# Performance work log

Hardware: AMD Instinct MI355X
Metric: run time of the kernel (lower is better)

Reference implementation:

```python
import jax, jax.numpy as jnp
import numpy as np

B, S, D = 2, 2048, 2048
H, Dh = 16, 128  # qkv_features = H*Dh = 2048
NEG = -1e10


def setup_inputs() -> dict:
    key = jax.random.key(0)
    k1, k2, k3 = jax.random.split(key, 3)
    x = jax.random.normal(k1, (B, S, D), dtype=jnp.float32)
    # variance_scaling(1.0, 'fan_in', 'normal') ~ std = 1/sqrt(fan_in)
    Wqkv = jax.random.normal(k2, (D, 3 * H * Dh), dtype=jnp.float32) / np.sqrt(D)
    bqkv = jnp.zeros((3 * H * Dh,), dtype=jnp.float32)
    Wout = jax.random.normal(k3, (H * Dh, D), dtype=jnp.float32) / np.sqrt(H * Dh)
    bout = jnp.zeros((D,), dtype=jnp.float32)
    return {"x": x, "Wqkv": Wqkv, "bqkv": bqkv, "Wout": Wout, "bout": bout}


def reference(x, Wqkv, bqkv, Wout, bout):
    b, s, _ = x.shape
    # fused QKV projection
    qkv = x @ Wqkv + bqkv                                   # [B, S, 3*H*Dh]
    qkv = qkv.reshape(b, s, 3, H, Dh).transpose(2, 0, 3, 1, 4)  # [3, B, H, S, Dh]
    q, k, v = qkv[0], qkv[1], qkv[2]
    scale = 1.0 / jnp.sqrt(jnp.asarray(Dh, dtype=x.dtype))
    # Each query chunk attends to the full key sequence with a causal mask,
    # which is mathematically full causal attention.
    scores = jnp.einsum('bhqd,bhkd->bhqk', q, k) * scale    # [B, H, S, S]
    causal = jnp.arange(s)[None, :] <= jnp.arange(s)[:, None]  # k <= q
    scores = jnp.where(causal[None, None, :, :], scores, NEG)
    weights = jax.nn.softmax(scores, axis=-1)
    out = jnp.einsum('bhqk,bhkd->bhqd', weights, v)         # [B, H, S, Dh]
    out = out.transpose(0, 2, 1, 3).reshape(b, s, H * Dh)
    return out @ Wout + bout
```

## Files before the change

### kernel.cpp

```cpp
#include <hip/hip_runtime.h>


typedef unsigned short u16;
typedef __attribute__((ext_vector_type(8))) short bf16x8;
typedef __attribute__((ext_vector_type(4))) float f32x4;

#define MFMA(a, b, c) __builtin_amdgcn_mfma_f32_16x16x32_bf16((a), (b), (c), 0, 0, 0)

__device__ __forceinline__ u16 f2bf(float f) {
    unsigned u = __builtin_bit_cast(unsigned, f);
    u += 0x7fffu + ((u >> 16) & 1u);
    return (u16)(u >> 16);
}

__device__ __forceinline__ void gload16(const void* g, void* l) {
    __builtin_amdgcn_global_load_lds(
        (const __attribute__((address_space(1))) void*)g,
        (__attribute__((address_space(3))) void*)l, 16, 0, 0);
}


__global__ __launch_bounds__(256) void k_cast(const float* __restrict__ src,
                                              u16* __restrict__ dst, int n4) {
    int i = blockIdx.x * 256 + threadIdx.x;
    if (i >= n4) return;
    float4 a = ((const float4*)src)[i];
    ushort4 r;
    r.x = f2bf(a.x); r.y = f2bf(a.y); r.z = f2bf(a.z); r.w = f2bf(a.w);
    ((ushort4*)dst)[i] = r;
}

__global__ __launch_bounds__(256) void k_castT(const float* __restrict__ src,
                                               u16* __restrict__ dst, int rows, int cols) {
    __shared__ float t[32][33];
    int c0 = blockIdx.x * 32, r0 = blockIdx.y * 32;
    int tx = threadIdx.x, ty = threadIdx.y;
#pragma unroll
    for (int i = 0; i < 4; ++i)
        t[ty + 8 * i][tx] = src[(size_t)(r0 + ty + 8 * i) * cols + (c0 + tx)];
    __syncthreads();
#pragma unroll
    for (int i = 0; i < 4; ++i)
        dst[(size_t)(c0 + ty + 8 * i) * rows + (r0 + tx)] = f2bf(t[tx][ty + 8 * i]);
}

__global__ __launch_bounds__(256) void k_transv(const u16* __restrict__ v,
                                                u16* __restrict__ vT) {
    __shared__ u16 t[32][33];
    int head = blockIdx.z;
    int s0 = blockIdx.x * 32, d0 = blockIdx.y * 32;
    const u16* vp = v + (size_t)head * 2048 * 128;
    u16* op = vT + (size_t)head * 128 * 2048;
    int tx = threadIdx.x, ty = threadIdx.y;
#pragma unroll
    for (int i = 0; i < 4; ++i)
        t[ty + 8 * i][tx] = vp[(size_t)(s0 + ty + 8 * i) * 128 + d0 + tx];
    __syncthreads();
#pragma unroll
    for (int i = 0; i < 4; ++i)
        op[(size_t)(d0 + ty + 8 * i) * 2048 + (s0 + tx)] = t[tx][ty + 8 * i];
}


template <int K>
__device__ __forceinline__ void gemm_core(const u16* __restrict__ A,
                                          const u16* __restrict__ BT,
                                          int m0, int n0,
                                          f32x4 (&acc)[4][4],
                                          u16* As, u16* Bs) {
    const int tid = threadIdx.x, wave = tid >> 6, lane = tid & 63;
    const int wr = (wave >> 1) * 64, wc = (wave & 1) * 64;
    for (int k0 = 0; k0 < K; k0 += 32) {
        __syncthreads();
#pragma unroll
        for (int i = 0; i < 2; ++i) {
            int cb = (i * 4 + wave) * 64;
            int c = cb + lane;
            int row = c >> 2, kk = (c & 3) * 8;
            gload16(A + (size_t)(m0 + row) * K + k0 + kk, As + cb * 8);
            gload16(BT + (size_t)(n0 + row) * K + k0 + kk, Bs + cb * 8);
        }
        __syncthreads();
        bf16x8 a[4], b[4];
#pragma unroll
        for (int m = 0; m < 4; ++m)
            a[m] = *(const bf16x8*)(As + (wr + m * 16 + (lane & 15)) * 32 + (lane >> 4) * 8);
#pragma unroll
        for (int n = 0; n < 4; ++n)
            b[n] = *(const bf16x8*)(Bs + (wc + n * 16 + (lane & 15)) * 32 + (lane >> 4) * 8);
        __builtin_amdgcn_s_setprio(1);
#pragma unroll
        for (int m = 0; m < 4; ++m)
#pragma unroll
            for (int n = 0; n < 4; ++n)
                acc[m][n] = MFMA(a[m], b[n], acc[m][n]);
        __builtin_amdgcn_s_setprio(0);
    }
}

__global__ __launch_bounds__(256) void k_gemm_qkv(const u16* __restrict__ A,
                                                  const u16* __restrict__ BT,
                                                  const float* __restrict__ bias,
                                                  u16* __restrict__ q,
                                                  u16* __restrict__ kbuf,
                                                  u16* __restrict__ v) {
    __shared__ __align__(16) u16 As[128 * 32];
    __shared__ __align__(16) u16 Bs[128 * 32];
    f32x4 acc[4][4] = {};
    const int orig = blockIdx.y * 48 + blockIdx.x;
    const int nb = (orig & 7) * 192 + (orig >> 3);
    const int m0 = (nb / 48) * 128, n0 = (nb % 48) * 128;
    gemm_core<2048>(A, BT, m0, n0, acc, As, Bs);

    const int tid = threadIdx.x, wave = tid >> 6, lane = tid & 63;
    const int wr = (wave >> 1) * 64, wc = (wave & 1) * 64;
    const int t = n0 >> 11;
    u16* dst = (t == 0) ? q : (t == 1) ? kbuf : v;
#pragma unroll
    for (int m = 0; m < 4; ++m)
#pragma unroll
        for (int n = 0; n < 4; ++n)
#pragma unroll
            for (int j = 0; j < 4; ++j) {
                int gr = m0 + wr + m * 16 + (lane >> 4) * 4 + j;
                int gc = n0 + wc + n * 16 + (lane & 15);
                float val = acc[m][n][j] + bias[gc];
                int bb = gr >> 11, s = gr & 2047;
                int rem = gc & 2047, h = rem >> 7, d = rem & 127;
                dst[((size_t)(bb * 16 + h) * 2048 + s) * 128 + d] = f2bf(val);
            }
}

__global__ __launch_bounds__(256) void k_gemm_out(const u16* __restrict__ A,
                                                  const u16* __restrict__ BT,
                                                  const float* __restrict__ bias,
                                                  float* __restrict__ out) {
    __shared__ __align__(16) u16 As[128 * 32];
    __shared__ __align__(16) u16 Bs[128 * 32];
    f32x4 acc[4][4] = {};
    const int orig = blockIdx.y * 16 + blockIdx.x;
    const int nb = (orig & 7) * 64 + (orig >> 3);
    const int m0 = (nb / 16) * 128, n0 = (nb % 16) * 128;
    gemm_core<2048>(A, BT, m0, n0, acc, As, Bs);

    const int tid = threadIdx.x, wave = tid >> 6, lane = tid & 63;
    const int wr = (wave >> 1) * 64, wc = (wave & 1) * 64;
#pragma unroll
    for (int m = 0; m < 4; ++m)
#pragma unroll
        for (int n = 0; n < 4; ++n)
#pragma unroll
            for (int j = 0; j < 4; ++j) {
                int gr = m0 + wr + m * 16 + (lane >> 4) * 4 + j;
                int gc = n0 + wc + n * 16 + (lane & 15);
                out[(size_t)gr * 2048 + gc] = acc[m][n][j] + bias[gc];
            }
}

__global__ __launch_bounds__(512) void k_attn(const u16* __restrict__ q,
                                              const u16* __restrict__ k,
                                              const u16* __restrict__ vT,
                                              u16* __restrict__ o) {
    __shared__ __align__(16) u16 KsA[2 * 64 * 128];
    __shared__ __align__(16) u16 VsA[2 * 128 * 64];
    __shared__ __align__(16) u16 PsA[8 * 16 * 64];
    char* ksB = (char*)KsA;
    char* vsB = (char*)VsA;

    const int tid = threadIdx.x, wave = tid >> 6, lane = tid & 63;
    char* psB = (char*)PsA + wave * 2048;

    const int lin = blockIdx.x;
    const int dd = (lin & 7) * 32 + (lin >> 3);
    const int head = dd >> 3, pair = dd & 7;

    const u16* qh = q + (size_t)head * 2048 * 128;
    const u16* kh = k + (size_t)head * 2048 * 128;
    const u16* vh = vT + (size_t)head * 128 * 2048;
    const int bb = head >> 4, hh = head & 15;
    const float qscale = 0.1275293562566334f;
    const float MFIX = 20.f;

    bf16x8 ones;
#pragma unroll
    for (int e = 0; e < 8; ++e) ones[e] = (short)0x3F80;

    auto stage = [&](int kv0, int bufsel) {
        char* kd = ksB + bufsel * 16384;
        char* vd = vsB + bufsel * 16384;
#pragma unroll
        for (int i = 0; i < 2; ++i) {
            int cb = (i * 8 + wave) * 64;
            int d = (cb + lane) * 16;
            int r = d >> 8;
            int co = (d & 255) ^ ((r & 7) << 4);
            gload16(kh + (size_t)(kv0 + r) * 128 + (co >> 1), kd + cb * 16);
        }
#pragma unroll
        for (int i = 0; i < 2; ++i) {
            int cb = (i * 8 + wave) * 64;
            int d = (cb + lane) * 16;
            int vr = d >> 7;
            int co = (d & 127) ^ ((vr & 7) << 4);
            gload16(vh + (size_t)vr * 2048 + kv0 + (co >> 1), vd + cb * 16);
        }
    };

#pragma unroll 1
    for (int qsel = 0; qsel < 2; ++qsel) {
        const int qi = qsel ? (15 - pair) : pair;
        const int q0 = qi * 128;
        const int ntile = 2 * qi + 2;

        bf16x8 qf[4];
        const int qr = q0 + wave * 16 + (lane & 15);
#pragma unroll
        for (int kt = 0; kt < 4; ++kt)
            qf[kt] = *(const bf16x8*)(qh + (size_t)qr * 128 + kt * 32 + (lane >> 4) * 8);

        f32x4 o_acc[8] = {};
        f32x4 l_r = {};

        stage(0, 0);
        int buf = 0;

#pragma unroll 1
        for (int t = 0; t < ntile; ++t) {
            const int kv0 = t * 64;
            if (t + 1 < ntile) {
                stage(kv0 + 64, buf ^ 1);
                asm volatile("s_waitcnt vmcnt(4)" ::: "memory");
            } else {
                asm volatile("s_waitcnt vmcnt(0)" ::: "memory");
            }
            __builtin_amdgcn_s_barrier();
            char* kb_ = ksB + buf * 16384;
            char* vb_ = vsB + buf * 16384;

            if (kv0 <= q0 + wave * 16 + 15) {
                f32x4 s_acc[4] = {};
                __builtin_amdgcn_s_setprio(1);
#pragma unroll
                for (int c = 0; c < 4; ++c) {
                    int row = c * 16 + (lane & 15);
#pragma unroll
                    for (int kt = 0; kt < 4; ++kt) {
                        bf16x8 kbf = *(const bf16x8*)(kb_ +
                            ((row * 256 + kt * 64 + (lane >> 4) * 16) ^ ((row & 7) << 4)));
                        s_acc[c] = MFMA(qf[kt], kbf, s_acc[c]);
                    }
                }
                __builtin_amdgcn_s_setprio(0);

                const bool maskblk = (kv0 + 64 > q0 + wave * 16);
#pragma unroll
                for (int j = 0; j < 4; ++j) {
                    int qg = q0 + wave * 16 + (lane >> 4) * 4 + j;
#pragma unroll
                    for (int c = 0; c < 4; ++c) {
                        float sv = fmaf(s_acc[c][j], qscale, -MFIX);
                        if (maskblk && (kv0 + c * 16 + (lane & 15)) > qg) sv = -1e30f;
                        s_acc[c][j] = exp2f(sv);
                    }
                }

#pragma unroll
                for (int c = 0; c < 4; ++c)
#pragma unroll
                    for (int j = 0; j < 4; ++j) {
                        int row = (lane >> 4) * 4 + j;
                        *(u16*)(psB + ((row * 128 + (c * 16 + (lane & 15)) * 2) ^ ((row & 7) << 4)))
                            = f2bf(s_acc[c][j]);
                    }
                bf16x8 pf[2];
#pragma unroll
                for (int kt = 0; kt < 2; ++kt) {
                    int row2 = lane & 15;
                    pf[kt] = *(const bf16x8*)(psB +
                        ((row2 * 128 + kt * 64 + (lane >> 4) * 16) ^ ((row2 & 7) << 4)));
                }

                __builtin_amdgcn_s_setprio(1);
                l_r = MFMA(pf[0], ones, l_r);
                l_r = MFMA(pf[1], ones, l_r);
#pragma unroll
                for (int c2 = 0; c2 < 8; ++c2) {
#pragma unroll
                    for (int kt = 0; kt < 2; ++kt) {
                        int row = c2 * 16 + (lane & 15);
                        bf16x8 vf = *(const bf16x8*)(vb_ +
                            ((row * 128 + kt * 64 + (lane >> 4) * 16) ^ ((row & 7) << 4)));
                        o_acc[c2] = MFMA(pf[kt], vf, o_acc[c2]);
                    }
                }
                __builtin_amdgcn_s_setprio(0);
            }

            __builtin_amdgcn_s_barrier();
            buf ^= 1;
        }

        float linv[4];
#pragma unroll
        for (int j = 0; j < 4; ++j) linv[j] = 1.0f / l_r[j];
#pragma unroll
        for (int c2 = 0; c2 < 8; ++c2)
#pragma unroll
            for (int j = 0; j < 4; ++j) {
                int qg = q0 + wave * 16 + (lane >> 4) * 4 + j;
                int d2 = c2 * 16 + (lane & 15);
                o[((size_t)(bb * 2048 + qg)) * 2048 + hh * 128 + d2]
                    = f2bf(o_acc[c2][j] * linv[j]);
            }
    }
}


extern "C" void kernel_launch(void* const* d_in, const int* in_sizes, int n_in,
                              void* d_out, int out_size, void* d_ws, size_t ws_size,
                              hipStream_t stream) {
    const float* x    = (const float*)d_in[0];
    const float* Wqkv = (const float*)d_in[1];
    const float* bqkv = (const float*)d_in[2];
    const float* Wout = (const float*)d_in[3];
    const float* bout = (const float*)d_in[4];
    float* out = (float*)d_out;

    char* ws = (char*)d_ws;
    const size_t SZ = 16777216;
    u16* q   = (u16*)(ws);
    u16* kb  = (u16*)(ws + SZ);
    u16* v   = (u16*)(ws + 2 * SZ);
    u16* vT  = (u16*)(ws + 3 * SZ);
    u16* ao  = v;
    u16* xb  = (u16*)(ws + 4 * SZ);
    u16* WqT = (u16*)(ws + 5 * SZ);
    u16* WoT = (u16*)(ws + 5 * SZ + 25165824);

    k_cast<<<dim3(8192), dim3(256), 0, stream>>>(x, xb, 2097152);
    k_castT<<<dim3(192, 64), dim3(32, 8), 0, stream>>>(Wqkv, WqT, 2048, 6144);
    k_castT<<<dim3(64, 64), dim3(32, 8), 0, stream>>>(Wout, WoT, 2048, 2048);
    k_gemm_qkv<<<dim3(48, 32), dim3(256), 0, stream>>>(xb, WqT, bqkv, q, kb, v);
    k_transv<<<dim3(64, 4, 32), dim3(32, 8), 0, stream>>>(v, vT);
    k_attn<<<dim3(256), dim3(512), 0, stream>>>(q, kb, vT, ao);
    k_gemm_out<<<dim3(16, 32), dim3(256), 0, stream>>>(ao, WoT, bout, out);
}
```

Measured before the change: 280.9 us.

## Switch attention kernel to 32x32x16 MFMA with 4 waves of 32 query rows

The attention kernel moves from 8 waves each handling 16 query rows with 16x16x32 MFMAs to 4 waves each handling 32 query rows with 32x32x16 MFMAs. K/V staging is redistributed over 4 waves and the P buffer is resized to match. The larger MFMA shape reuses each LDS operand fragment across more output, cutting LDS reads per FLOP, but halves the waves per block and raises register pressure, which may reduce latency hiding. A trivial index reorder in k_transv is included.

```diff
diff --git a/kernel.cpp b/kernel.cpp
--- a/kernel.cpp
+++ b/kernel.cpp
@@ -4,8 +4,10 @@
 typedef unsigned short u16;
 typedef __attribute__((ext_vector_type(8))) short bf16x8;
 typedef __attribute__((ext_vector_type(4))) float f32x4;
-
-#define MFMA(a, b, c) __builtin_amdgcn_mfma_f32_16x16x32_bf16((a), (b), (c), 0, 0, 0)
+typedef __attribute__((ext_vector_type(16))) float f32x16;
+
+#define MFMA(a, b, c)   __builtin_amdgcn_mfma_f32_16x16x32_bf16((a), (b), (c), 0, 0, 0)
+#define MFMA32(a, b, c) __builtin_amdgcn_mfma_f32_32x32x16_bf16((a), (b), (c), 0, 0, 0)
 
 __device__ __forceinline__ u16 f2bf(float f) {
     unsigned u = __builtin_bit_cast(unsigned, f);
@@ -58,7 +60,7 @@
     __syncthreads();
 #pragma unroll
     for (int i = 0; i < 4; ++i)
-        op[(size_t)(d0 + ty + 8 * i) * 2048 + (s0 + tx)] = t[tx][ty + 8 * i];
+        op[(size_t)(d0 + 8 * i + ty) * 2048 + (s0 + tx)] = t[tx][ty + 8 * i];
 }
 
 
@@ -157,18 +159,19 @@
             }
 }
 
-__global__ __launch_bounds__(512) void k_attn(const u16* __restrict__ q,
+__global__ __launch_bounds__(256) void k_attn(const u16* __restrict__ q,
                                               const u16* __restrict__ k,
                                               const u16* __restrict__ vT,
                                               u16* __restrict__ o) {
     __shared__ __align__(16) u16 KsA[2 * 64 * 128];
     __shared__ __align__(16) u16 VsA[2 * 128 * 64];
-    __shared__ __align__(16) u16 PsA[8 * 16 * 64];
+    __shared__ __align__(16) u16 PsA[4 * 32 * 64];
     char* ksB = (char*)KsA;
     char* vsB = (char*)VsA;
 
     const int tid = threadIdx.x, wave = tid >> 6, lane = tid & 63;
-    char* psB = (char*)PsA + wave * 2048;
+    char* psB = (char*)PsA + wave * 4096;
+    const int ln31 = lane & 31, lhi = lane >> 5;
 
     const int lin = blockIdx.x;
     const int dd = (lin & 7) * 32 + (lin >> 3);
@@ -189,16 +192,16 @@
         char* kd = ksB + bufsel * 16384;
         char* vd = vsB + bufsel * 16384;
 #pragma unroll
-        for (int i = 0; i < 2; ++i) {
-            int cb = (i * 8 + wave) * 64;
+        for (int i = 0; i < 4; ++i) {
+            int cb = (i * 4 + wave) * 64;
             int d = (cb + lane) * 16;
             int r = d >> 8;
             int co = (d & 255) ^ ((r & 7) << 4);
             gload16(kh + (size_t)(kv0 + r) * 128 + (co >> 1), kd + cb * 16);
         }
 #pragma unroll
-        for (int i = 0; i < 2; ++i) {
-            int cb = (i * 8 + wave) * 64;
+        for (int i = 0; i < 4; ++i) {
+            int cb = (i * 4 + wave) * 64;
             int d = (cb + lane) * 16;
             int vr = d >> 7;
             int co = (d & 127) ^ ((vr & 7) << 4);
@@ -212,14 +215,14 @@
         const int q0 = qi * 128;
         const int ntile = 2 * qi + 2;
 
-        bf16x8 qf[4];
-        const int qr = q0 + wave * 16 + (lane & 15);
-#pragma unroll
-        for (int kt = 0; kt < 4; ++kt)
-            qf[kt] = *(const bf16x8*)(qh + (size_t)qr * 128 + kt * 32 + (lane >> 4) * 8);
-
-        f32x4 o_acc[8] = {};
-        f32x4 l_r = {};
+        bf16x8 qf[8];
+        const int qr = q0 + wave * 32 + ln31;
+#pragma unroll
+        for (int kt = 0; kt < 8; ++kt)
+            qf[kt] = *(const bf16x8*)(qh + (size_t)qr * 128 + kt * 16 + lhi * 8);
+
+        f32x16 o_acc[4] = {};
+        f32x16 l_acc = {};
 
         stage(0, 0);
         int buf = 0;
@@ -229,7 +232,7 @@
             const int kv0 = t * 64;
             if (t + 1 < ntile) {
                 stage(kv0 + 64, buf ^ 1);
-                asm volatile("s_waitcnt vmcnt(4)" ::: "memory");
+                asm volatile("s_waitcnt vmcnt(8)" ::: "memory");
             } else {
                 asm volatile("s_waitcnt vmcnt(0)" ::: "memory");
             }
@@ -237,60 +240,53 @@
             char* kb_ = ksB + buf * 16384;
             char* vb_ = vsB + buf * 16384;
 
-            if (kv0 <= q0 + wave * 16 + 15) {
-                f32x4 s_acc[4] = {};
+            if (kv0 <= q0 + wave * 32 + 31) {
+                f32x16 s_acc[2] = {};
                 __builtin_amdgcn_s_setprio(1);
 #pragma unroll
-                for (int c = 0; c < 4; ++c) {
-                    int row = c * 16 + (lane & 15);
-#pragma unroll
-                    for (int kt = 0; kt < 4; ++kt) {
+                for (int c = 0; c < 2; ++c) {
+                    int row = c * 32 + ln31;
+#pragma unroll
+                    for (int kt = 0; kt < 8; ++kt) {
                         bf16x8 kbf = *(const bf16x8*)(kb_ +
-                            ((row * 256 + kt * 64 + (lane >> 4) * 16) ^ ((row & 7) << 4)));
-                        s_acc[c] = MFMA(qf[kt], kbf, s_acc[c]);
+                            ((row * 256 + kt * 32 + lhi * 16) ^ ((row & 7) << 4)));
+                        s_acc[c] = MFMA32(qf[kt], kbf, s_acc[c]);
                     }
                 }
                 __builtin_amdgcn_s_setprio(0);
 
-                const bool maskblk = (kv0 + 64 > q0 + wave * 16);
-#pragma unroll
-                for (int j = 0; j < 4; ++j) {
-                    int qg = q0 + wave * 16 + (lane >> 4) * 4 + j;
-#pragma unroll
-                    for (int c = 0; c < 4; ++c) {
-                        float sv = fmaf(s_acc[c][j], qscale, -MFIX);
-                        if (maskblk && (kv0 + c * 16 + (lane & 15)) > qg) sv = -1e30f;
-                        s_acc[c][j] = exp2f(sv);
+                const bool maskblk = (kv0 + 64 > q0 + wave * 32);
+#pragma unroll
+                for (int c = 0; c < 2; ++c)
+#pragma unroll
+                    for (int r = 0; r < 16; ++r) {
+                        int ql = (r & 3) + 8 * (r >> 2) + 4 * lhi;
+                        float sv = fmaf(s_acc[c][r], qscale, -MFIX);
+                        if (maskblk && (kv0 + c * 32 + ln31) > (q0 + wave * 32 + ql))
+                            sv = -1e30f;
+                        float p = exp2f(sv);
+                        *(u16*)(psB + ((ql * 128 + (c * 32 + ln31) * 2) ^ ((ql & 7) << 4)))
+                            = f2bf(p);
                     }
-                }
-
-#pragma unroll
-                for (int c = 0; c < 4; ++c)
-#pragma unroll
-                    for (int j = 0; j < 4; ++j) {
-                        int row = (lane >> 4) * 4 + j;
-                        *(u16*)(psB + ((row * 128 + (c * 16 + (lane & 15)) * 2) ^ ((row & 7) << 4)))
-                            = f2bf(s_acc[c][j]);
-                    }
-                bf16x8 pf[2];
-#pragma unroll
-                for (int kt = 0; kt < 2; ++kt) {
-                    int row2 = lane & 15;
-                    pf[kt] = *(const bf16x8*)(psB +
-                        ((row2 * 128 + kt * 64 + (lane >> 4) * 16) ^ ((row2 & 7) << 4)));
-                }
+
+                bf16x8 pf[4];
+#pragma unroll
+                for (int ks = 0; ks < 4; ++ks)
+                    pf[ks] = *(const bf16x8*)(psB +
+                        ((ln31 * 128 + ks * 32 + lhi * 16) ^ ((lane & 7) << 4)));
 
                 __builtin_amdgcn_s_setprio(1);
-                l_r = MFMA(pf[0], ones, l_r);
-                l_r = MFMA(pf[1], ones, l_r);
-#pragma unroll
-                for (int c2 = 0; c2 < 8; ++c2) {
-#pragma unroll
-                    for (int kt = 0; kt < 2; ++kt) {
-                        int row = c2 * 16 + (lane & 15);
+#pragma unroll
+                for (int ks = 0; ks < 4; ++ks)
+                    l_acc = MFMA32(pf[ks], ones, l_acc);
+#pragma unroll
+                for (int nd = 0; nd < 4; ++nd) {
+                    int row = nd * 32 + ln31;
+#pragma unroll
+                    for (int ks = 0; ks < 4; ++ks) {
                         bf16x8 vf = *(const bf16x8*)(vb_ +
-                            ((row * 128 + kt * 64 + (lane >> 4) * 16) ^ ((row & 7) << 4)));
-                        o_acc[c2] = MFMA(pf[kt], vf, o_acc[c2]);
+                            ((row * 128 + ks * 32 + lhi * 16) ^ ((row & 7) << 4)));
+                        o_acc[nd] = MFMA32(pf[ks], vf, o_acc[nd]);
                     }
                 }
                 __builtin_amdgcn_s_setprio(0);
@@ -300,17 +296,17 @@
             buf ^= 1;
         }
 
-        float linv[4];
-#pragma unroll
-        for (int j = 0; j < 4; ++j) linv[j] = 1.0f / l_r[j];
-#pragma unroll
-        for (int c2 = 0; c2 < 8; ++c2)
-#pragma unroll
-            for (int j = 0; j < 4; ++j) {
-                int qg = q0 + wave * 16 + (lane >> 4) * 4 + j;
-                int d2 = c2 * 16 + (lane & 15);
+        float linv[16];
+#pragma unroll
+        for (int r = 0; r < 16; ++r) linv[r] = 1.0f / l_acc[r];
+#pragma unroll
+        for (int nd = 0; nd < 4; ++nd)
+#pragma unroll
+            for (int r = 0; r < 16; ++r) {
+                int qg = q0 + wave * 32 + (r & 3) + 8 * (r >> 2) + 4 * lhi;
+                int d2 = nd * 32 + ln31;
                 o[((size_t)(bb * 2048 + qg)) * 2048 + hh * 128 + d2]
-                    = f2bf(o_acc[c2][j] * linv[j]);
+                    = f2bf(o_acc[nd][r] * linv[r]);
             }
     }
 }
@@ -342,6 +338,6 @@
     k_castT<<<dim3(64, 64), dim3(32, 8), 0, stream>>>(Wout, WoT, 2048, 2048);
     k_gemm_qkv<<<dim3(48, 32), dim3(256), 0, stream>>>(xb, WqT, bqkv, q, kb, v);
     k_transv<<<dim3(64, 4, 32), dim3(32, 8), 0, stream>>>(v, vT);
-    k_attn<<<dim3(256), dim3(512), 0, stream>>>(q, kb, vT, ao);
+    k_attn<<<dim3(256), dim3(256), 0, stream>>>(q, kb, vT, ao);
     k_gemm_out<<<dim3(16, 32), dim3(256), 0, stream>>>(ao, WoT, bout, out);
 }
```

Result: slower. 293.6 us (+4.5%).

## Use K=64 tiles with XOR-swizzled LDS in QKV projection GEMM

Applied to the files above, without the earlier changes.

Adds a gemm_core64 variant that loads 64-wide K slices per iteration, halving the number of barrier pairs per K loop, and applies an XOR swizzle to LDS addresses to avoid bank conflicts on fragment reads. The QKV projection kernel switches to it, doubling its shared memory tiles. It costs more LDS per block, which may reduce occupancy. The only other change reorders index terms in the V transpose and has no effect.

```diff
diff --git a/kernel.cpp b/kernel.cpp
--- a/kernel.cpp
+++ b/kernel.cpp
@@ -58,7 +58,7 @@
     __syncthreads();
 #pragma unroll
     for (int i = 0; i < 4; ++i)
-        op[(size_t)(d0 + ty + 8 * i) * 2048 + (s0 + tx)] = t[tx][ty + 8 * i];
+        op[(size_t)(d0 + 8 * i + ty) * 2048 + (s0 + tx)] = t[tx][ty + 8 * i];
 }
 
 
@@ -98,19 +98,71 @@
     }
 }
 
+
+template <int K>
+__device__ __forceinline__ void gemm_core64(const u16* __restrict__ A,
+                                            const u16* __restrict__ BT,
+                                            int m0, int n0,
+                                            f32x4 (&acc)[4][4],
+                                            u16* As, u16* Bs) {
+    const int tid = threadIdx.x, wave = tid >> 6, lane = tid & 63;
+    const int wr = (wave >> 1) * 64, wc = (wave & 1) * 64;
+    char* AsB = (char*)As;
+    char* BsB = (char*)Bs;
+    for (int k0 = 0; k0 < K; k0 += 64) {
+        __syncthreads();
+#pragma unroll
+        for (int i = 0; i < 4; ++i) {
+            int cb = (i * 4 + wave) * 64;
+            int d = (cb + lane) * 16;
+            int row = d >> 7;
+            int co = (d & 127) ^ ((row & 7) << 4);
+            gload16(A + (size_t)(m0 + row) * K + k0 + (co >> 1), AsB + cb * 16);
+            gload16(BT + (size_t)(n0 + row) * K + k0 + (co >> 1), BsB + cb * 16);
+        }
+        __syncthreads();
+        bf16x8 a[2][4], b[2][4];
+#pragma unroll
+        for (int ks = 0; ks < 2; ++ks)
+#pragma unroll
+            for (int m = 0; m < 4; ++m) {
+                int row = wr + m * 16 + (lane & 15);
+                a[ks][m] = *(const bf16x8*)(AsB +
+                    ((row * 128 + ks * 64 + (lane >> 4) * 16) ^ ((row & 7) << 4)));
+            }
+#pragma unroll
+        for (int ks = 0; ks < 2; ++ks)
+#pragma unroll
+            for (int n = 0; n < 4; ++n) {
+                int row = wc + n * 16 + (lane & 15);
+                b[ks][n] = *(const bf16x8*)(BsB +
+                    ((row * 128 + ks * 64 + (lane >> 4) * 16) ^ ((row & 7) << 4)));
+            }
+        __builtin_amdgcn_s_setprio(1);
+#pragma unroll
+        for (int ks = 0; ks < 2; ++ks)
+#pragma unroll
+            for (int m = 0; m < 4; ++m)
+#pragma unroll
+                for (int n = 0; n < 4; ++n)
+                    acc[m][n] = MFMA(a[ks][m], b[ks][n], acc[m][n]);
+        __builtin_amdgcn_s_setprio(0);
+    }
+}
+
 __global__ __launch_bounds__(256) void k_gemm_qkv(const u16* __restrict__ A,
                                                   const u16* __restrict__ BT,
                                                   const float* __restrict__ bias,
                                                   u16* __restrict__ q,
                                                   u16* __restrict__ kbuf,
                                                   u16* __restrict__ v) {
-    __shared__ __align__(16) u16 As[128 * 32];
-    __shared__ __align__(16) u16 Bs[128 * 32];
+    __shared__ __align__(16) u16 As[128 * 64];
+    __shared__ __align__(16) u16 Bs[128 * 64];
     f32x4 acc[4][4] = {};
     const int orig = blockIdx.y * 48 + blockIdx.x;
     const int nb = (orig & 7) * 192 + (orig >> 3);
     const int m0 = (nb / 48) * 128, n0 = (nb % 48) * 128;
-    gemm_core<2048>(A, BT, m0, n0, acc, As, Bs);
+    gemm_core64<2048>(A, BT, m0, n0, acc, As, Bs);
 
     const int tid = threadIdx.x, wave = tid >> 6, lane = tid & 63;
     const int wr = (wave >> 1) * 64, wc = (wave & 1) * 64;
```

Measured after the change: 272.8 us. -2.9%, faster.
